# Optimization experiments

Hardware: AMD Instinct MI355X
Metric: run time of the kernel (lower is better)

Reference implementation:

```python
import jax, jax.numpy as jnp
import numpy as np

N_EMBD = 2048
N_HEAD = 16
N_INNER = 8192
EPS = 1e-5


def _wn_weight(v, g):
    # torch weight_norm with dim=1 on weight [out, in]:
    # w[:, j] = g[j] * v[:, j] / ||v[:, j]||_2
    norm = jnp.sqrt(jnp.sum(v * v, axis=0))  # [in]
    return v * (g / norm)[None, :]


def _layer_norm(x, gamma, beta):
    mu = jnp.mean(x, axis=-1, keepdims=True)
    var = jnp.mean(jnp.square(x - mu), axis=-1, keepdims=True)
    return (x - mu) * jax.lax.rsqrt(var + EPS) * gamma + beta


def setup_inputs() -> dict:
    key = jax.random.key(0)
    ks = jax.random.split(key, 12)
    E, I, H = N_EMBD, N_INNER, N_HEAD
    s = lambda n: 1.0 / np.sqrt(n)
    return {
        "hidden_states": jax.random.normal(ks[0], (2, 2048, E), jnp.float32),
        "ln1_g": jnp.ones((E,), jnp.float32),
        "ln1_b": jnp.zeros((E,), jnp.float32),
        "w_qkv": jax.random.normal(ks[1], (3 * E, E), jnp.float32) * s(E),
        "b_qkv": jnp.zeros((3 * E,), jnp.float32),
        "attn_proj_v": jax.random.normal(ks[2], (E, E), jnp.float32) * s(E),
        "attn_proj_g": jnp.abs(jax.random.normal(ks[3], (E,), jnp.float32)) + 0.5,
        "attn_proj_b": jnp.zeros((E,), jnp.float32),
        "emotion_bias": jax.random.normal(ks[4], (H,), jnp.float32) * 0.1,
        "ln2_g": jnp.ones((E,), jnp.float32),
        "ln2_b": jnp.zeros((E,), jnp.float32),
        "w_fc": jax.random.normal(ks[5], (I, E), jnp.float32) * s(E),
        "b_fc": jnp.zeros((I,), jnp.float32),
        "mlp_proj_v": jax.random.normal(ks[6], (E, I), jnp.float32) * s(I),
        "mlp_proj_g": jnp.abs(jax.random.normal(ks[7], (I,), jnp.float32)) + 0.5,
        "mlp_proj_b": jnp.zeros((E,), jnp.float32),
    }


def reference(hidden_states, ln1_g, ln1_b, w_qkv, b_qkv, attn_proj_v, attn_proj_g,
              attn_proj_b, emotion_bias, ln2_g, ln2_b, w_fc, b_fc,
              mlp_proj_v, mlp_proj_g, mlp_proj_b):
    B, S, E = hidden_states.shape
    H = N_HEAD
    D = E // H

    # --- attention sub-block ---
    residual = hidden_states
    x = _layer_norm(hidden_states, ln1_g, ln1_b)
    qkv = x @ w_qkv.T + b_qkv                       # [B,S,3E]
    q, k, v = jnp.split(qkv, 3, axis=-1)
    q = q.reshape(B, S, H, D).transpose(0, 2, 1, 3)  # [B,H,S,D]
    k = k.reshape(B, S, H, D).transpose(0, 2, 1, 3)
    v = v.reshape(B, S, H, D).transpose(0, 2, 1, 3)

    scores = jnp.einsum("bhqd,bhkd->bhqk", q, k) / jnp.sqrt(jnp.float32(D))
    scores = scores + emotion_bias[None, :, None, None]
    probs = jax.nn.softmax(scores, axis=-1)
    attn = jnp.einsum("bhqk,bhkd->bhqd", probs, v)   # [B,H,S,D]
    attn = attn.transpose(0, 2, 1, 3).reshape(B, S, E)
    w_proj = _wn_weight(attn_proj_v, attn_proj_g)
    attn = attn @ w_proj.T + attn_proj_b

    hidden = attn + residual

    # --- MLP sub-block ---
    residual = hidden
    x = _layer_norm(hidden, ln2_g, ln2_b)
    h = jax.nn.gelu(x @ w_fc.T + b_fc, approximate=False)
    w_proj2 = _wn_weight(mlp_proj_v, mlp_proj_g)
    h = h @ w_proj2.T + mlp_proj_b
    return residual + h
```

## Files before the change

kernel.cpp:

```cpp
#include <hip/hip_runtime.h>
#include <hip/hip_bf16.h>

#define DEVI __device__ __forceinline__

typedef __attribute__((ext_vector_type(8))) __bf16 bf16x8;
typedef __attribute__((ext_vector_type(4))) float f32x4;
typedef __attribute__((ext_vector_type(4))) unsigned short u16x4;
typedef __attribute__((ext_vector_type(8))) unsigned short u16x8;

DEVI unsigned short f2bf(float f) {
  unsigned int u = __float_as_uint(f);
  u += 0x7FFFu + ((u >> 16) & 1u);
  return (unsigned short)(u >> 16);
}
DEVI float bf2f(unsigned short u) {
  return __uint_as_float(((unsigned int)u) << 16);
}

#define GLD16(g, l) __builtin_amdgcn_global_load_lds(                      \
    (const __attribute__((address_space(1))) void*)(g),                    \
    (__attribute__((address_space(3))) void*)(l), 16, 0, 0)


__global__ __launch_bounds__(256) void cast_k(const float* __restrict__ in,
                                              unsigned short* __restrict__ out,
                                              int n4) {
  for (int i = blockIdx.x * 256 + threadIdx.x; i < n4; i += gridDim.x * 256) {
    f32x4 v = ((const f32x4*)in)[i];
    u16x4 o;
    o.x = f2bf(v.x); o.y = f2bf(v.y); o.z = f2bf(v.z); o.w = f2bf(v.w);
    ((u16x4*)out)[i] = o;
  }
}

__global__ __launch_bounds__(256) void colnorm1_k(const float* __restrict__ v,
                                                  float* __restrict__ part,
                                                  int cols) {
  const int tid = threadIdx.x;
  const int g = tid & 127;
  const int s = tid >> 7;
  const int c0 = blockIdx.x * 512;
  const int r0 = blockIdx.y * 64 + s * 32;
  const float* base = v + (size_t)r0 * cols + c0 + g * 4;
  f32x4 acc = {};
#pragma unroll 4
  for (int i = 0; i < 32; ++i) {
    f32x4 x = *(const f32x4*)(base + (size_t)i * cols);
    acc.x += x.x * x.x; acc.y += x.y * x.y;
    acc.z += x.z * x.z; acc.w += x.w * x.w;
  }
  __shared__ f32x4 red[256];
  red[tid] = acc;
  __syncthreads();
  if (s == 0) {
    f32x4 a = red[tid], b = red[tid + 128];
    f32x4 o;
    o.x = a.x + b.x; o.y = a.y + b.y; o.z = a.z + b.z; o.w = a.w + b.w;
    *(f32x4*)(part + (size_t)blockIdx.y * cols + c0 + g * 4) = o;
  }
}

__global__ __launch_bounds__(256) void colnorm2_k(const float* __restrict__ part,
                                                  const float* __restrict__ g,
                                                  float* __restrict__ s,
                                                  int cols, int nrc) {
  const int c = blockIdx.x * 256 + threadIdx.x;
  float acc = 0.f;
  for (int i = 0; i < nrc; ++i) acc += part[(size_t)i * cols + c];
  s[c] = g[c] * rsqrtf(acc);
}

__global__ __launch_bounds__(256) void scale_cast_k(const float* __restrict__ in,
                                                    const float* __restrict__ s,
                                                    unsigned short* __restrict__ out,
                                                    int cols, int n4) {
  const int cmask4 = (cols >> 2) - 1;
  for (int i = blockIdx.x * 256 + threadIdx.x; i < n4; i += gridDim.x * 256) {
    f32x4 v = ((const f32x4*)in)[i];
    f32x4 sv = ((const f32x4*)s)[i & cmask4];
    u16x4 o;
    o.x = f2bf(v.x * sv.x); o.y = f2bf(v.y * sv.y);
    o.z = f2bf(v.z * sv.z); o.w = f2bf(v.w * sv.w);
    ((u16x4*)out)[i] = o;
  }
}

__global__ __launch_bounds__(256) void ln_k(const float* __restrict__ x,
                                            const float* __restrict__ g,
                                            const float* __restrict__ b,
                                            unsigned short* __restrict__ out) {
  const int tid = threadIdx.x, lane = tid & 63, wid = tid >> 6;
  const int row = blockIdx.x;
  const float* xr = x + (size_t)row * 2048;
  f32x4 a0 = ((const f32x4*)xr)[tid];
  f32x4 a1 = ((const f32x4*)xr)[tid + 256];
  float s = a0.x + a0.y + a0.z + a0.w + a1.x + a1.y + a1.z + a1.w;
  float ss = a0.x * a0.x + a0.y * a0.y + a0.z * a0.z + a0.w * a0.w +
             a1.x * a1.x + a1.y * a1.y + a1.z * a1.z + a1.w * a1.w;
#pragma unroll
  for (int m = 1; m < 64; m <<= 1) {
    s += __shfl_xor(s, m);
    ss += __shfl_xor(ss, m);
  }
  __shared__ float red[8];
  if (lane == 0) { red[wid] = s; red[4 + wid] = ss; }
  __syncthreads();
  s = red[0] + red[1] + red[2] + red[3];
  ss = red[4] + red[5] + red[6] + red[7];
  const float mu = s * (1.f / 2048.f);
  const float var = ss * (1.f / 2048.f) - mu * mu;
  const float rs = rsqrtf(var + 1e-5f);
  f32x4 g0 = ((const f32x4*)g)[tid], g1 = ((const f32x4*)g)[tid + 256];
  f32x4 b0 = ((const f32x4*)b)[tid], b1 = ((const f32x4*)b)[tid + 256];
  u16x4 o0, o1;
  o0.x = f2bf((a0.x - mu) * rs * g0.x + b0.x);
  o0.y = f2bf((a0.y - mu) * rs * g0.y + b0.y);
  o0.z = f2bf((a0.z - mu) * rs * g0.z + b0.z);
  o0.w = f2bf((a0.w - mu) * rs * g0.w + b0.w);
  o1.x = f2bf((a1.x - mu) * rs * g1.x + b1.x);
  o1.y = f2bf((a1.y - mu) * rs * g1.y + b1.y);
  o1.z = f2bf((a1.z - mu) * rs * g1.z + b1.z);
  o1.w = f2bf((a1.w - mu) * rs * g1.w + b1.w);
  unsigned short* orow = out + (size_t)row * 2048;
  *(u16x4*)(orow + 4 * tid) = o0;
  *(u16x4*)(orow + 1024 + 4 * tid) = o1;
}

__global__ __launch_bounds__(256) void vtrans_k(const unsigned short* __restrict__ qkv,
                                                unsigned short* __restrict__ vt) {
  __shared__ unsigned short t[64][134];
  const int tid = threadIdx.x;
  const int bh = blockIdx.x >> 5, st = blockIdx.x & 31;
  const int b = bh >> 4, h = bh & 15;
  const unsigned short* vb = qkv + (size_t)(b * 2048 + st * 64) * 6144 + 4096 + h * 128;
#pragma unroll
  for (int i = 0; i < 4; ++i) {
    int f = tid + (i << 8);
    int row = f >> 4, c8 = f & 15;
    u16x8 x = *(const u16x8*)(vb + (size_t)row * 6144 + c8 * 8);
#pragma unroll
    for (int j = 0; j < 4; ++j) {
      unsigned int pk = ((unsigned int)x[2 * j + 1] << 16) | x[2 * j];
      *(unsigned int*)&t[row][c8 * 8 + 2 * j] = pk;
    }
  }
  __syncthreads();
  const int lane = tid & 63, wid = tid >> 6;
  unsigned short* ob = vt + ((size_t)bh << 18) + (st << 6);
#pragma unroll
  for (int j = 0; j < 32; ++j) {
    int d = (wid << 5) + j;
    ob[((size_t)d << 11) + lane] = t[lane][d];
  }
}

__global__ __launch_bounds__(256) void g4red_k(const unsigned short* __restrict__ parts,
                                               const float* __restrict__ bias,
                                               const float* __restrict__ res,
                                               float* __restrict__ out, int n4) {
  const size_t PS = (size_t)4096 * 2048;
  for (int i = blockIdx.x * 256 + threadIdx.x; i < n4; i += gridDim.x * 256) {
    u16x4 a = ((const u16x4*)(parts))[i];
    u16x4 b = ((const u16x4*)(parts + PS))[i];
    f32x4 r = ((const f32x4*)res)[i];
    f32x4 bb = ((const f32x4*)bias)[i & 511];
    f32x4 o;
    o.x = bf2f(a.x) + bf2f(b.x) + r.x + bb.x;
    o.y = bf2f(a.y) + bf2f(b.y) + r.y + bb.y;
    o.z = bf2f(a.z) + bf2f(b.z) + r.z + bb.z;
    o.w = bf2f(a.w) + bf2f(b.w) + r.w + bb.w;
    ((f32x4*)out)[i] = o;
  }
}

struct GemmP {
  const unsigned short* A;
  const unsigned short* B;
  const float* bias;
  const float* res;
  float* outF;
  unsigned short* outH;
  int M, N, K;
};

template <int EPI>
DEVI void gemm128_body(const GemmP& p, int m0, int n0, int k0, int nk) {
  const int tid = threadIdx.x, lane = tid & 63, wid = tid >> 6;
  const int K = p.K;
  const int wr = wid >> 1, wc = wid & 1;

  __shared__ __align__(16) unsigned short sA[2][4096];
  __shared__ __align__(16) unsigned short sB[2][4096];

  const int c0 = tid, c1 = tid + 256;
  const unsigned short* gA0 = p.A + (size_t)(m0 + (c0 >> 2)) * K + k0 + ((c0 & 3) << 3);
  const unsigned short* gA1 = p.A + (size_t)(m0 + (c1 >> 2)) * K + k0 + ((c1 & 3) << 3);
  const unsigned short* gB0 = p.B + (size_t)(n0 + (c0 >> 2)) * K + k0 + ((c0 & 3) << 3);
  const unsigned short* gB1 = p.B + (size_t)(n0 + (c1 >> 2)) * K + k0 + ((c1 & 3) << 3);
  const int l0 = wid << 9, l1 = (wid << 9) + 2048;

  f32x4 acc[4][4] = {};
  const int arow = (wr << 6) + (lane & 15);
  const int brow = (wc << 6) + (lane & 15);
  const int koff = (lane >> 4) << 3;

#define STAGE128(bufi, t) do { int ko = (t) << 5;       \
    GLD16(gA0 + ko, &sA[bufi][l0]);                     \
    GLD16(gA1 + ko, &sA[bufi][l1]);                     \
    GLD16(gB0 + ko, &sB[bufi][l0]);                     \
    GLD16(gB1 + ko, &sB[bufi][l1]); } while (0)

  STAGE128(0, 0);
  __syncthreads();
  int cur = 0;
  for (int t = 0; t < nk; ++t) {
    if (t + 1 < nk) STAGE128(cur ^ 1, t + 1);
    bf16x8 af[4], bfr[4];
#pragma unroll
    for (int i = 0; i < 4; ++i)
      af[i] = *(const bf16x8*)&sA[cur][(arow + (i << 4)) * 32 + koff];
#pragma unroll
    for (int i = 0; i < 4; ++i)
      bfr[i] = *(const bf16x8*)&sB[cur][(brow + (i << 4)) * 32 + koff];
#pragma unroll
    for (int i = 0; i < 4; ++i)
#pragma unroll
      for (int j = 0; j < 4; ++j)
        acc[i][j] = __builtin_amdgcn_mfma_f32_16x16x32_bf16(af[i], bfr[j], acc[i][j], 0, 0, 0);
    __syncthreads();
    cur ^= 1;
  }
#undef STAGE128

  const int rbase = m0 + (wr << 6) + ((lane >> 4) << 2);
  const int cbase = n0 + (wc << 6) + (lane & 15);
#pragma unroll
  for (int mi = 0; mi < 4; ++mi) {
#pragma unroll
    for (int ni = 0; ni < 4; ++ni) {
      const int col = cbase + (ni << 4);
#pragma unroll
      for (int r = 0; r < 4; ++r) {
        const int row = rbase + (mi << 4) + r;
        if constexpr (EPI == 0) {
          p.outH[(size_t)row * p.N + col] = f2bf(acc[mi][ni][r] + p.bias[col]);
        } else if constexpr (EPI == 1) {
          const size_t o = (size_t)row * p.N + col;
          p.outF[o] = acc[mi][ni][r] + p.bias[col] + p.res[o];
        } else {
          p.outH[(size_t)row * p.N + col] = f2bf(acc[mi][ni][r]);
        }
      }
    }
  }
}

__global__ __launch_bounds__(256) void g1_qkv128(GemmP p) {
  const int x = blockIdx.x & 7, i = blockIdx.x >> 3;
  const int bm = i & 31;
  const int bn = x * 6 + (i >> 5);
  gemm128_body<0>(p, bm << 7, bn << 7, 0, p.K >> 5);
}
__global__ __launch_bounds__(256) void g2_proj128(GemmP p) {
  const int x = blockIdx.x & 7, i = blockIdx.x >> 3;
  const int bm = (x >> 1) * 8 + (i >> 3);
  const int bn = (x & 1) * 8 + (i & 7);
  gemm128_body<1>(p, bm << 7, bn << 7, 0, p.K >> 5);
}
__global__ __launch_bounds__(256) void g4_splitk(GemmP p) {
  const int x = blockIdx.x & 7, i = blockIdx.x >> 3;
  const int ks = i & 1, j = i >> 1;
  const int bm = (x >> 1) * 8 + (j >> 3);
  const int bn = (x & 1) * 8 + (j & 7);
  GemmP q = p;
  q.outH = p.outH + (size_t)ks * 4096 * 2048;
  gemm128_body<5>(q, bm << 7, bn << 7, ks << 12, 128);
}

DEVI void setup256(const GemmP& p, int m0, int n0,
                   const unsigned short*& gsA0, const unsigned short*& gsA1,
                   const unsigned short*& gsB0, const unsigned short*& gsB1) {
  const int tid = threadIdx.x;
  int r_[2], c_[2];
#pragma unroll
  for (int j = 0; j < 2; ++j) {
    int d = tid * 16 + j * 8192;
    int w = (d & 1023) ^ (((d >> 9) & 1) << 5);
    r_[j] = ((d >> 10) << 4) + (w >> 6);
    c_[j] = (w & 63) >> 1;
  }
  gsA0 = p.A + (size_t)(m0 + r_[0]) * p.K + c_[0];
  gsA1 = p.A + (size_t)(m0 + r_[1]) * p.K + c_[1];
  gsB0 = p.B + (size_t)(n0 + r_[0]) * p.K + c_[0];
  gsB1 = p.B + (size_t)(n0 + r_[1]) * p.K + c_[1];
}

DEVI void epi256g(const GemmP& p, f32x4 (&acc)[8][4], int m0, int n0) {
  const int lane = threadIdx.x & 63, wid = threadIdx.x >> 6;
  const int wr = wid >> 2, wc = wid & 3;
  const int lr = lane & 15, lk = lane >> 4;
  const int rbase = m0 + wr * 128 + (lk << 2);
  const int cbase = n0 + wc * 64 + lr;
#pragma unroll
  for (int m = 0; m < 8; ++m) {
#pragma unroll
    for (int n = 0; n < 4; ++n) {
      const int col = cbase + (n << 4);
      const float bb = p.bias[col];
#pragma unroll
      for (int r = 0; r < 4; ++r) {
        const int row = rbase + (m << 4) + r;
        float v = acc[m][n][r] + bb;
        float y = 0.7978845608028654f * (v + 0.044715f * v * v * v);
        float u = __expf(2.f * y);
        float gl = (y > 40.f) ? v : v * (u / (u + 1.f));
        p.outH[(size_t)row * p.N + col] = f2bf(gl);
      }
    }
  }
}

DEVI void gemm8p_body(const GemmP& p, unsigned short* lds_raw, int m0, int n0) {
  const int tid = threadIdx.x, lane = tid & 63, wid = tid >> 6;
  const int wr = wid >> 2, wc = wid & 3;
  const int lr = lane & 15, lk = lane >> 4;
  const int fb = (lr * 64 + lk * 16) ^ ((lr & 8) << 2);

  const unsigned short *gsA0, *gsA1, *gsB0, *gsB1;
  setup256(p, m0, n0, gsA0, gsA1, gsB0, gsB1);

#define STAGE_A8(b, kt) do { unsigned short* _d = lds_raw + ((b) << 14);       \
    GLD16(gsA0 + ((size_t)(kt) << 5), _d + (tid << 3));                        \
    GLD16(gsA1 + ((size_t)(kt) << 5), _d + 4096 + (tid << 3)); } while (0)
#define STAGE_B8(b, kt) do { unsigned short* _d = lds_raw + ((b) << 14) + 8192;\
    GLD16(gsB0 + ((size_t)(kt) << 5), _d + (tid << 3));                        \
    GLD16(gsB1 + ((size_t)(kt) << 5), _d + 4096 + (tid << 3)); } while (0)

  f32x4 acc[8][4] = {};
  const int NK = p.K >> 5;

  STAGE_A8(0, 0); STAGE_B8(0, 0);
  STAGE_A8(1, 1); STAGE_B8(1, 1);
  STAGE_A8(2, 2); STAGE_B8(2, 2);
  asm volatile("s_waitcnt vmcnt(8)" ::: "memory");
  __builtin_amdgcn_s_barrier();

  for (int t = 0; t < NK; ++t) {
    const int bi = t & 3;
    const char* tA = (const char*)(lds_raw + (bi << 14));
    const char* tB = (const char*)(lds_raw + (bi << 14) + 8192);
    bf16x8 a_[4], b_[4];
#pragma unroll
    for (int n = 0; n < 4; ++n)
      b_[n] = *(const bf16x8*)(tB + (((wc << 2) + n) << 10) + fb);
#pragma unroll
    for (int m = 0; m < 4; ++m)
      a_[m] = *(const bf16x8*)(tA + (((wr << 3) + m) << 10) + fb);
    if (t + 3 < NK) STAGE_A8((t + 3) & 3, t + 3);
    __builtin_amdgcn_s_barrier();
    asm volatile("s_waitcnt lgkmcnt(0)" ::: "memory");
    __builtin_amdgcn_sched_barrier(0);
    __builtin_amdgcn_s_setprio(1);
#pragma unroll
    for (int m = 0; m < 4; ++m)
#pragma unroll
      for (int n = 0; n < 4; ++n)
        acc[m][n] = __builtin_amdgcn_mfma_f32_16x16x32_bf16(a_[m], b_[n], acc[m][n], 0, 0, 0);
    __builtin_amdgcn_s_setprio(0);
    __builtin_amdgcn_s_barrier();
#pragma unroll
    for (int m = 0; m < 4; ++m)
      a_[m] = *(const bf16x8*)(tA + (((wr << 3) + 4 + m) << 10) + fb);
    if (t + 3 < NK) STAGE_B8((t + 3) & 3, t + 3);
    if (t + 3 < NK)      asm volatile("s_waitcnt vmcnt(8)" ::: "memory");
    else if (t + 2 < NK) asm volatile("s_waitcnt vmcnt(4)" ::: "memory");
    else if (t + 1 < NK) asm volatile("s_waitcnt vmcnt(0)" ::: "memory");
    __builtin_amdgcn_s_barrier();
    asm volatile("s_waitcnt lgkmcnt(0)" ::: "memory");
    __builtin_amdgcn_sched_barrier(0);
    __builtin_amdgcn_s_setprio(1);
#pragma unroll
    for (int m = 0; m < 4; ++m)
#pragma unroll
      for (int n = 0; n < 4; ++n)
        acc[4 + m][n] = __builtin_amdgcn_mfma_f32_16x16x32_bf16(a_[m], b_[n], acc[4 + m][n], 0, 0, 0);
    __builtin_amdgcn_s_setprio(0);
    __builtin_amdgcn_s_barrier();
  }
#undef STAGE_A8
#undef STAGE_B8
  epi256g(p, acc, m0, n0);
}

DEVI void gemm2p_body(const GemmP& p, unsigned short* lds_raw, int m0, int n0) {
  const int tid = threadIdx.x, lane = tid & 63, wid = tid >> 6;
  const int wr = wid >> 2, wc = wid & 3;
  const int lr = lane & 15, lk = lane >> 4;
  const int fb = (lr * 64 + lk * 16) ^ ((lr & 8) << 2);

  const unsigned short *gsA0, *gsA1, *gsB0, *gsB1;
  setup256(p, m0, n0, gsA0, gsA1, gsB0, gsB1);

#define STG2(b, kt) do { unsigned short* _d = lds_raw + ((b) << 14);     \
    GLD16(gsA0 + ((size_t)(kt) << 5), _d + (tid << 3));                  \
    GLD16(gsA1 + ((size_t)(kt) << 5), _d + 4096 + (tid << 3));           \
    GLD16(gsB0 + ((size_t)(kt) << 5), _d + 8192 + (tid << 3));           \
    GLD16(gsB1 + ((size_t)(kt) << 5), _d + 12288 + (tid << 3)); } while (0)

  f32x4 acc[8][4] = {};
  const int NK = p.K >> 5;
  STG2(0, 0);
  __syncthreads();
  int cur = 0;
  for (int t = 0; t < NK; ++t) {
    if (t + 1 < NK) STG2(cur ^ 1, t + 1);
    const char* tA = (const char*)(lds_raw + (cur << 14));
    const char* tB = tA + 16384;
    bf16x8 a_[8], b_[4];
#pragma unroll
    for (int n = 0; n < 4; ++n)
      b_[n] = *(const bf16x8*)(tB + (((wc << 2) + n) << 10) + fb);
#pragma unroll
    for (int m = 0; m < 8; ++m)
      a_[m] = *(const bf16x8*)(tA + (((wr << 3) + m) << 10) + fb);
#pragma unroll
    for (int m = 0; m < 8; ++m)
#pragma unroll
      for (int n = 0; n < 4; ++n)
        acc[m][n] = __builtin_amdgcn_mfma_f32_16x16x32_bf16(a_[m], b_[n], acc[m][n], 0, 0, 0);
    __syncthreads();
    cur ^= 1;
  }
#undef STG2
  epi256g(p, acc, m0, n0);
}

__global__ __launch_bounds__(512, 2) void g3a_fc8p(GemmP p) {
  extern __shared__ unsigned short lds_raw[];
  const int x = blockIdx.x & 7, i = blockIdx.x >> 3;
  const int bm = (x >> 2) * 4 + (i >> 3);
  const int bn = (x & 3) * 8 + (i & 7);
  gemm8p_body(p, lds_raw, bm << 8, bn << 8);
}
__global__ __launch_bounds__(512, 2) void g3b_fc2p(GemmP p) {
  extern __shared__ unsigned short lds_raw[];
  const int x = blockIdx.x & 7, i = blockIdx.x >> 3;
  const int bm = (x >> 2) * 4 + (i >> 3);
  const int bn = (x & 3) * 8 + (i & 7);
  gemm2p_body(p, lds_raw, 2048 + (bm << 8), bn << 8);
}

__global__ __launch_bounds__(512) void attn_k(const unsigned short* __restrict__ qkv,
                                              const unsigned short* __restrict__ Vt,
                                              unsigned short* __restrict__ O) {
  const int tid = threadIdx.x, lane = tid & 63, wid = tid >> 6;
  const int bid = blockIdx.x;
  const int pos = bid >> 3;
  const int bh = (bid & 7) * 4 + (pos >> 4);
  const int qt = pos & 15;
  const int q0 = qt * 128 + wid * 16;
  const int b = bh >> 4, h = bh & 15;

  __shared__ __align__(16) unsigned short sK[64 * 128];
  __shared__ __align__(16) unsigned short sV[128 * 64];
  __shared__ __align__(16) unsigned short sP[8][16 * 68];

  const unsigned short* Qb = qkv + (size_t)(b * 2048) * 6144 + h * 128;
  const unsigned short* Kb = qkv + (size_t)(b * 2048) * 6144 + 2048 + h * 128;
  const unsigned short* Vb = Vt + ((size_t)bh << 18);

  bf16x8 qf[4];
  {
    const unsigned short* qp = Qb + (size_t)(q0 + (lane & 15)) * 6144 + ((lane >> 4) << 3);
#pragma unroll
    for (int kk = 0; kk < 4; ++kk) qf[kk] = *(const bf16x8*)(qp + kk * 32);
  }

  int koffs[2], voffs[2];
#pragma unroll
  for (int i = 0; i < 2; ++i) {
    const int c = tid + (i << 9);
    const int kv = c >> 4, jj = c & 15;
    const int js = (jj & 8) | ((jj ^ kv) & 7);
    koffs[i] = kv * 6144 + (js << 3);
    const int d = c >> 3, j2 = c & 7;
    const int js2 = j2 ^ (d & 7);
    voffs[i] = d * 2048 + (js2 << 3);
  }
  u16x8 kreg[2], vreg[2];
  auto PREF = [&](int kt) {
    const int kv0 = kt << 6;
    const unsigned short* kb = Kb + (size_t)kv0 * 6144;
#pragma unroll
    for (int i = 0; i < 2; ++i) {
      kreg[i] = *(const u16x8*)(kb + koffs[i]);
      vreg[i] = *(const u16x8*)(Vb + kv0 + voffs[i]);
    }
  };

  f32x4 oacc[8] = {};
  float mrun = -3e38f, lrun = 0.f;
  PREF(0);

  for (int kt = 0; kt < 32; ++kt) {
#pragma unroll
    for (int i = 0; i < 2; ++i) {
      const int c8 = (tid + (i << 9)) << 3;
      *(u16x8*)&sK[c8] = kreg[i];
      *(u16x8*)&sV[c8] = vreg[i];
    }
    __syncthreads();
    if (kt + 1 < 32) PREF(kt + 1);

    f32x4 sc[4] = {};
    __builtin_amdgcn_s_setprio(1);
#pragma unroll
    for (int ti = 0; ti < 4; ++ti) {
#pragma unroll
      for (int kk = 0; kk < 4; ++kk) {
        const int row = (ti << 4) + (lane & 15);
        int bo = (row << 8) + (kk << 6) + ((lane >> 4) << 4);
        bo ^= (row & 7) << 4;
        bf16x8 kf = *(const bf16x8*)((const char*)sK + bo);
        sc[ti] = __builtin_amdgcn_mfma_f32_16x16x32_bf16(kf, qf[kk], sc[ti], 0, 0, 0);
      }
    }
    __builtin_amdgcn_s_setprio(0);

    float pv[16];
    float mx = -3e38f;
#pragma unroll
    for (int ti = 0; ti < 4; ++ti)
#pragma unroll
      for (int r = 0; r < 4; ++r) {
        float x = sc[ti][r] * 0.08838834764831845f;
        pv[(ti << 2) + r] = x;
        mx = fmaxf(mx, x);
      }
    mx = fmaxf(mx, __shfl_xor(mx, 16));
    mx = fmaxf(mx, __shfl_xor(mx, 32));

    float corr = 1.f;
    if (!__all(mx - mrun <= 8.f)) {
      const float mnew = fmaxf(mrun, mx);
      corr = __expf(mrun - mnew);
      mrun = mnew;
      float fr[4];
#pragma unroll
      for (int r = 0; r < 4; ++r) fr[r] = __shfl(corr, ((lane >> 4) << 2) + r);
#pragma unroll
      for (int di = 0; di < 8; ++di)
#pragma unroll
        for (int r = 0; r < 4; ++r) oacc[di][r] *= fr[r];
    }
    float psum = 0.f;
#pragma unroll
    for (int i2 = 0; i2 < 16; ++i2) {
      float e = __expf(pv[i2] - mrun);
      pv[i2] = e;
      psum += e;
    }
    psum += __shfl_xor(psum, 16);
    psum += __shfl_xor(psum, 32);
    lrun = lrun * corr + psum;

    unsigned short* prow = &sP[wid][(lane & 15) * 68];
#pragma unroll
    for (int ti = 0; ti < 4; ++ti) {
      u16x4 w4;
      w4.x = f2bf(pv[(ti << 2) + 0]);
      w4.y = f2bf(pv[(ti << 2) + 1]);
      w4.z = f2bf(pv[(ti << 2) + 2]);
      w4.w = f2bf(pv[(ti << 2) + 3]);
      *(u16x4*)&prow[(ti << 4) + ((lane >> 4) << 2)] = w4;
    }

    __builtin_amdgcn_s_setprio(1);
#pragma unroll
    for (int di = 0; di < 8; ++di) {
#pragma unroll
      for (int ks = 0; ks < 2; ++ks) {
        bf16x8 pf = *(const bf16x8*)((const char*)&sP[wid][0] +
                                     (lane & 15) * 136 + (ks << 6) + ((lane >> 4) << 4));
        const int dr = (di << 4) + (lane & 15);
        int bo = (dr << 7) + (ks << 6) + ((lane >> 4) << 4);
        bo ^= (dr & 7) << 4;
        bf16x8 vf = *(const bf16x8*)((const char*)sV + bo);
        oacc[di] = __builtin_amdgcn_mfma_f32_16x16x32_bf16(pf, vf, oacc[di], 0, 0, 0);
      }
    }
    __builtin_amdgcn_s_setprio(0);
    __syncthreads();
  }

  float il[4];
#pragma unroll
  for (int r = 0; r < 4; ++r) il[r] = 1.f / __shfl(lrun, ((lane >> 4) << 2) + r);
  const size_t obase = ((size_t)(b * 2048 + q0)) * 2048 + h * 128;
#pragma unroll
  for (int di = 0; di < 8; ++di)
#pragma unroll
    for (int r = 0; r < 4; ++r) {
      const size_t o = obase + (size_t)(((lane >> 4) << 2) + r) * 2048 + (di << 4) + (lane & 15);
      O[o] = f2bf(oacc[di][r] * il[r]);
    }
}


extern "C" void kernel_launch(void* const* d_in, const int* in_sizes, int n_in,
                              void* d_out, int out_size, void* d_ws, size_t ws_size,
                              hipStream_t stream) {
  (void)in_sizes; (void)n_in; (void)out_size; (void)ws_size;
  const float* hidden = (const float*)d_in[0];
  const float* ln1_g = (const float*)d_in[1];
  const float* ln1_b = (const float*)d_in[2];
  const float* w_qkv = (const float*)d_in[3];
  const float* b_qkv = (const float*)d_in[4];
  const float* apv = (const float*)d_in[5];
  const float* apg = (const float*)d_in[6];
  const float* apb = (const float*)d_in[7];
  const float* ln2_g = (const float*)d_in[9];
  const float* ln2_b = (const float*)d_in[10];
  const float* w_fc = (const float*)d_in[11];
  const float* b_fc = (const float*)d_in[12];
  const float* mpv = (const float*)d_in[13];
  const float* mpg = (const float*)d_in[14];
  const float* mpb = (const float*)d_in[15];

  char* w = (char*)d_ws;
  const size_t MBs = 1ull << 20;
  unsigned short* xln = (unsigned short*)(w + 0);
  float* hidden2 = (float*)(w + 0);
  unsigned short* vtbuf = (unsigned short*)(w + 32 * MBs);
  unsigned short* hbuf = (unsigned short*)(w + 32 * MBs);
  unsigned short* qkv = (unsigned short*)(w + 96 * MBs);
  unsigned short* wfc_bf = (unsigned short*)(w + 96 * MBs);
  unsigned short* partH = (unsigned short*)(w + 96 * MBs);
  unsigned short* xln2 = (unsigned short*)(w + 128 * MBs);
  unsigned short* attn_out = (unsigned short*)(w + 144 * MBs);
  unsigned short* wqkv_bf = (unsigned short*)(w + 160 * MBs);
  unsigned short* w2_bf = (unsigned short*)(w + 160 * MBs);
  unsigned short* wproj_bf = (unsigned short*)(w + 192 * MBs);
  float* s_attn = (float*)(w + 200 * MBs);
  float* s_mlp = (float*)(w + 200 * MBs + 32768);
  float* part_attn = (float*)(w + 201 * MBs);
  float* part_mlp = (float*)(w + 202 * MBs);

  hipFuncSetAttribute((const void*)g3a_fc8p, hipFuncAttributeMaxDynamicSharedMemorySize, 131072);
  hipFuncSetAttribute((const void*)g3b_fc2p, hipFuncAttributeMaxDynamicSharedMemorySize, 65536);

  cast_k<<<2048, 256, 0, stream>>>(w_qkv, wqkv_bf, (6144 * 2048) / 4);
  colnorm1_k<<<dim3(4, 32), 256, 0, stream>>>(apv, part_attn, 2048);
  colnorm2_k<<<8, 256, 0, stream>>>(part_attn, apg, s_attn, 2048, 32);
  scale_cast_k<<<2048, 256, 0, stream>>>(apv, s_attn, wproj_bf, 2048, (2048 * 2048) / 4);
  colnorm1_k<<<dim3(16, 32), 256, 0, stream>>>(mpv, part_mlp, 8192);
  colnorm2_k<<<32, 256, 0, stream>>>(part_mlp, mpg, s_mlp, 8192, 32);

  ln_k<<<4096, 256, 0, stream>>>(hidden, ln1_g, ln1_b, xln);

  GemmP p1 = {xln, wqkv_bf, b_qkv, nullptr, nullptr, qkv, 4096, 6144, 2048};
  g1_qkv128<<<1536, 256, 0, stream>>>(p1);

  vtrans_k<<<1024, 256, 0, stream>>>(qkv, vtbuf);

  attn_k<<<512, 512, 0, stream>>>(qkv, vtbuf, attn_out);

  cast_k<<<2048, 256, 0, stream>>>(w_fc, wfc_bf, (8192 * 2048) / 4);
  scale_cast_k<<<4096, 256, 0, stream>>>(mpv, s_mlp, w2_bf, 8192, (2048 * 8192) / 4);

  GemmP p2 = {attn_out, wproj_bf, apb, hidden, hidden2, nullptr, 4096, 2048, 2048};
  g2_proj128<<<512, 256, 0, stream>>>(p2);

  ln_k<<<4096, 256, 0, stream>>>(hidden2, ln2_g, ln2_b, xln2);

  GemmP p3 = {xln2, wfc_bf, b_fc, nullptr, nullptr, hbuf, 4096, 8192, 2048};
  g3a_fc8p<<<256, 512, 131072, stream>>>(p3);
  g3b_fc2p<<<256, 512, 65536, stream>>>(p3);

  GemmP p4 = {hbuf, w2_bf, mpb, nullptr, nullptr, partH, 4096, 2048, 8192};
  g4_splitk<<<1024, 256, 0, stream>>>(p4);
  g4red_k<<<2048, 256, 0, stream>>>(partH, mpb, hidden2, (float*)d_out,
                                    (4096 * 2048) / 4);
}
```

Before: 895.5 us.

## Move QKV and MLP-down GEMMs to 256x256 tile kernel with 4-way split-K

The QKV projection and the second MLP GEMM now use the larger 256x256, 512-thread double-buffered GEMM body instead of the 128x128 kernel. The MLP-down GEMM's split-K goes from 2 to 4 slices, and the reduction kernel now sums four bf16 partial buffers. The aim is more data reuse per tile and fewer, larger blocks. In exchange, the reduction pass reads twice as much partial data, and the partial buffers need more workspace, which may overlap other buffers.

```diff
diff --git a/kernel.cpp b/kernel.cpp
--- a/kernel.cpp
+++ b/kernel.cpp
@@ -162,13 +162,15 @@
   for (int i = blockIdx.x * 256 + threadIdx.x; i < n4; i += gridDim.x * 256) {
     u16x4 a = ((const u16x4*)(parts))[i];
     u16x4 b = ((const u16x4*)(parts + PS))[i];
+    u16x4 c = ((const u16x4*)(parts + 2 * PS))[i];
+    u16x4 d = ((const u16x4*)(parts + 3 * PS))[i];
     f32x4 r = ((const f32x4*)res)[i];
     f32x4 bb = ((const f32x4*)bias)[i & 511];
     f32x4 o;
-    o.x = bf2f(a.x) + bf2f(b.x) + r.x + bb.x;
-    o.y = bf2f(a.y) + bf2f(b.y) + r.y + bb.y;
-    o.z = bf2f(a.z) + bf2f(b.z) + r.z + bb.z;
-    o.w = bf2f(a.w) + bf2f(b.w) + r.w + bb.w;
+    o.x = bf2f(a.x) + bf2f(b.x) + bf2f(c.x) + bf2f(d.x) + r.x + bb.x;
+    o.y = bf2f(a.y) + bf2f(b.y) + bf2f(c.y) + bf2f(d.y) + r.y + bb.y;
+    o.z = bf2f(a.z) + bf2f(b.z) + bf2f(c.z) + bf2f(d.z) + r.z + bb.z;
+    o.w = bf2f(a.w) + bf2f(b.w) + bf2f(c.w) + bf2f(d.w) + r.w + bb.w;
     ((f32x4*)out)[i] = o;
   }
 }
@@ -183,7 +185,6 @@
   int M, N, K;
 };
 
-template <int EPI>
 DEVI void gemm128_body(const GemmP& p, int m0, int n0, int k0, int nk) {
   const int tid = threadIdx.x, lane = tid & 63, wid = tid >> 6;
   const int K = p.K;
@@ -242,42 +243,21 @@
 #pragma unroll
       for (int r = 0; r < 4; ++r) {
         const int row = rbase + (mi << 4) + r;
-        if constexpr (EPI == 0) {
-          p.outH[(size_t)row * p.N + col] = f2bf(acc[mi][ni][r] + p.bias[col]);
-        } else if constexpr (EPI == 1) {
-          const size_t o = (size_t)row * p.N + col;
-          p.outF[o] = acc[mi][ni][r] + p.bias[col] + p.res[o];
-        } else {
-          p.outH[(size_t)row * p.N + col] = f2bf(acc[mi][ni][r]);
-        }
+        const size_t o = (size_t)row * p.N + col;
+        p.outF[o] = acc[mi][ni][r] + p.bias[col] + p.res[o];
       }
     }
   }
 }
 
-__global__ __launch_bounds__(256) void g1_qkv128(GemmP p) {
-  const int x = blockIdx.x & 7, i = blockIdx.x >> 3;
-  const int bm = i & 31;
-  const int bn = x * 6 + (i >> 5);
-  gemm128_body<0>(p, bm << 7, bn << 7, 0, p.K >> 5);
-}
 __global__ __launch_bounds__(256) void g2_proj128(GemmP p) {
   const int x = blockIdx.x & 7, i = blockIdx.x >> 3;
   const int bm = (x >> 1) * 8 + (i >> 3);
   const int bn = (x & 1) * 8 + (i & 7);
-  gemm128_body<1>(p, bm << 7, bn << 7, 0, p.K >> 5);
-}
-__global__ __launch_bounds__(256) void g4_splitk(GemmP p) {
-  const int x = blockIdx.x & 7, i = blockIdx.x >> 3;
-  const int ks = i & 1, j = i >> 1;
-  const int bm = (x >> 1) * 8 + (j >> 3);
-  const int bn = (x & 1) * 8 + (j & 7);
-  GemmP q = p;
-  q.outH = p.outH + (size_t)ks * 4096 * 2048;
-  gemm128_body<5>(q, bm << 7, bn << 7, ks << 12, 128);
-}
-
-DEVI void setup256(const GemmP& p, int m0, int n0,
+  gemm128_body(p, bm << 7, bn << 7, 0, p.K >> 5);
+}
+
+DEVI void setup256(const GemmP& p, int m0, int n0, int k0,
                    const unsigned short*& gsA0, const unsigned short*& gsA1,
                    const unsigned short*& gsB0, const unsigned short*& gsB1) {
   const int tid = threadIdx.x;
@@ -289,13 +269,15 @@
     r_[j] = ((d >> 10) << 4) + (w >> 6);
     c_[j] = (w & 63) >> 1;
   }
-  gsA0 = p.A + (size_t)(m0 + r_[0]) * p.K + c_[0];
-  gsA1 = p.A + (size_t)(m0 + r_[1]) * p.K + c_[1];
-  gsB0 = p.B + (size_t)(n0 + r_[0]) * p.K + c_[0];
-  gsB1 = p.B + (size_t)(n0 + r_[1]) * p.K + c_[1];
-}
-
-DEVI void epi256g(const GemmP& p, f32x4 (&acc)[8][4], int m0, int n0) {
+  gsA0 = p.A + (size_t)(m0 + r_[0]) * p.K + k0 + c_[0];
+  gsA1 = p.A + (size_t)(m0 + r_[1]) * p.K + k0 + c_[1];
+  gsB0 = p.B + (size_t)(n0 + r_[0]) * p.K + k0 + c_[0];
+  gsB1 = p.B + (size_t)(n0 + r_[1]) * p.K + k0 + c_[1];
+}
+
+template <int EPI>
+DEVI void epi256(const GemmP& p, f32x4 (&acc)[8][4], int m0, int n0,
+                 unsigned short* outH) {
   const int lane = threadIdx.x & 63, wid = threadIdx.x >> 6;
   const int wr = wid >> 2, wc = wid & 3;
   const int lr = lane & 15, lk = lane >> 4;
@@ -306,15 +288,17 @@
 #pragma unroll
     for (int n = 0; n < 4; ++n) {
       const int col = cbase + (n << 4);
-      const float bb = p.bias[col];
+      const float bb = (EPI == 5) ? 0.f : p.bias[col];
 #pragma unroll
       for (int r = 0; r < 4; ++r) {
         const int row = rbase + (m << 4) + r;
         float v = acc[m][n][r] + bb;
-        float y = 0.7978845608028654f * (v + 0.044715f * v * v * v);
-        float u = __expf(2.f * y);
-        float gl = (y > 40.f) ? v : v * (u / (u + 1.f));
-        p.outH[(size_t)row * p.N + col] = f2bf(gl);
+        if constexpr (EPI == 2) {
+          float y = 0.7978845608028654f * (v + 0.044715f * v * v * v);
+          float u = __expf(2.f * y);
+          v = (y > 40.f) ? v : v * (u / (u + 1.f));
+        }
+        outH[(size_t)row * p.N + col] = f2bf(v);
       }
     }
   }
@@ -327,7 +311,7 @@
   const int fb = (lr * 64 + lk * 16) ^ ((lr & 8) << 2);
 
   const unsigned short *gsA0, *gsA1, *gsB0, *gsB1;
-  setup256(p, m0, n0, gsA0, gsA1, gsB0, gsB1);
+  setup256(p, m0, n0, 0, gsA0, gsA1, gsB0, gsB1);
 
 #define STAGE_A8(b, kt) do { unsigned short* _d = lds_raw + ((b) << 14);       \
     GLD16(gsA0 + ((size_t)(kt) << 5), _d + (tid << 3));                        \
@@ -389,17 +373,19 @@
   }
 #undef STAGE_A8
 #undef STAGE_B8
-  epi256g(p, acc, m0, n0);
-}
-
-DEVI void gemm2p_body(const GemmP& p, unsigned short* lds_raw, int m0, int n0) {
+  epi256<2>(p, acc, m0, n0, p.outH);
+}
+
+template <int EPI>
+DEVI void gemm2p_body(const GemmP& p, unsigned short* lds_raw, int m0, int n0,
+                      int k0, int nk, unsigned short* outH) {
   const int tid = threadIdx.x, lane = tid & 63, wid = tid >> 6;
   const int wr = wid >> 2, wc = wid & 3;
   const int lr = lane & 15, lk = lane >> 4;
   const int fb = (lr * 64 + lk * 16) ^ ((lr & 8) << 2);
 
   const unsigned short *gsA0, *gsA1, *gsB0, *gsB1;
-  setup256(p, m0, n0, gsA0, gsA1, gsB0, gsB1);
+  setup256(p, m0, n0, k0, gsA0, gsA1, gsB0, gsB1);
 
 #define STG2(b, kt) do { unsigned short* _d = lds_raw + ((b) << 14);     \
     GLD16(gsA0 + ((size_t)(kt) << 5), _d + (tid << 3));                  \
@@ -408,12 +394,11 @@
     GLD16(gsB1 + ((size_t)(kt) << 5), _d + 12288 + (tid << 3)); } while (0)
 
   f32x4 acc[8][4] = {};
-  const int NK = p.K >> 5;
   STG2(0, 0);
   __syncthreads();
   int cur = 0;
-  for (int t = 0; t < NK; ++t) {
-    if (t + 1 < NK) STG2(cur ^ 1, t + 1);
+  for (int t = 0; t < nk; ++t) {
+    if (t + 1 < nk) STG2(cur ^ 1, t + 1);
     const char* tA = (const char*)(lds_raw + (cur << 14));
     const char* tB = tA + 16384;
     bf16x8 a_[8], b_[4];
@@ -432,9 +417,16 @@
     cur ^= 1;
   }
 #undef STG2
-  epi256g(p, acc, m0, n0);
-}
-
+  epi256<EPI>(p, acc, m0, n0, outH);
+}
+
+__global__ __launch_bounds__(512, 2) void g1_qkv256(GemmP p) {
+  extern __shared__ unsigned short lds_raw[];
+  const int x = blockIdx.x & 7, i = blockIdx.x >> 3;
+  const int bm = (x & 1) * 8 + (i & 7);
+  const int bn = (x >> 1) * 6 + (i >> 3);
+  gemm2p_body<0>(p, lds_raw, bm << 8, bn << 8, 0, p.K >> 5, p.outH);
+}
 __global__ __launch_bounds__(512, 2) void g3a_fc8p(GemmP p) {
   extern __shared__ unsigned short lds_raw[];
   const int x = blockIdx.x & 7, i = blockIdx.x >> 3;
@@ -447,7 +439,16 @@
   const int x = blockIdx.x & 7, i = blockIdx.x >> 3;
   const int bm = (x >> 2) * 4 + (i >> 3);
   const int bn = (x & 3) * 8 + (i & 7);
-  gemm2p_body(p, lds_raw, 2048 + (bm << 8), bn << 8);
+  gemm2p_body<2>(p, lds_raw, 2048 + (bm << 8), bn << 8, 0, p.K >> 5, p.outH);
+}
+__global__ __launch_bounds__(512, 2) void g4_splitk256(GemmP p) {
+  extern __shared__ unsigned short lds_raw[];
+  const int x = blockIdx.x & 7, i = blockIdx.x >> 3;
+  const int ks = x & 3;
+  const int bm = (x >> 2) * 8 + (i >> 3);
+  const int bn = i & 7;
+  unsigned short* outH = p.outH + (size_t)ks * 4096 * 2048;
+  gemm2p_body<5>(p, lds_raw, bm << 8, bn << 8, ks << 11, 64, outH);
 }
 
 __global__ __launch_bounds__(512) void attn_k(const unsigned short* __restrict__ qkv,
@@ -646,8 +647,10 @@
   float* part_attn = (float*)(w + 201 * MBs);
   float* part_mlp = (float*)(w + 202 * MBs);
 
+  hipFuncSetAttribute((const void*)g1_qkv256, hipFuncAttributeMaxDynamicSharedMemorySize, 65536);
   hipFuncSetAttribute((const void*)g3a_fc8p, hipFuncAttributeMaxDynamicSharedMemorySize, 131072);
   hipFuncSetAttribute((const void*)g3b_fc2p, hipFuncAttributeMaxDynamicSharedMemorySize, 65536);
+  hipFuncSetAttribute((const void*)g4_splitk256, hipFuncAttributeMaxDynamicSharedMemorySize, 65536);
 
   cast_k<<<2048, 256, 0, stream>>>(w_qkv, wqkv_bf, (6144 * 2048) / 4);
   colnorm1_k<<<dim3(4, 32), 256, 0, stream>>>(apv, part_attn, 2048);
@@ -659,7 +662,7 @@
   ln_k<<<4096, 256, 0, stream>>>(hidden, ln1_g, ln1_b, xln);
 
   GemmP p1 = {xln, wqkv_bf, b_qkv, nullptr, nullptr, qkv, 4096, 6144, 2048};
-  g1_qkv128<<<1536, 256, 0, stream>>>(p1);
+  g1_qkv256<<<384, 512, 65536, stream>>>(p1);
 
   vtrans_k<<<1024, 256, 0, stream>>>(qkv, vtbuf);
 
@@ -678,7 +681,7 @@
   g3b_fc2p<<<256, 512, 65536, stream>>>(p3);
 
   GemmP p4 = {hbuf, w2_bf, mpb, nullptr, nullptr, partH, 4096, 2048, 8192};
-  g4_splitk<<<1024, 256, 0, stream>>>(p4);
+  g4_splitk256<<<512, 512, 65536, stream>>>(p4);
   g4red_k<<<2048, 256, 0, stream>>>(partH, mpb, hidden2, (float*)d_out,
                                     (4096 * 2048) / 4);
 }
```

After: 862.5 us. 3.7% less time.
